# Optimization experiments

Measured on AMD Instinct MI355X. Metric: run time of the kernel, lower is better.

Reference implementation:

```python
import jax, jax.numpy as jnp
import numpy as np

EPS = 1e-5  # haiku LayerNorm default
BIG = 1e9


def layernorm(x, scale, offset):
    mu = jnp.mean(x, axis=-1, keepdims=True)
    var = jnp.var(x, axis=-1, keepdims=True)
    return scale * (x - mu) * jax.lax.rsqrt(var + EPS) + offset


def setup_inputs() -> dict:
    key = jax.random.key(0)
    ks = iter(jax.random.split(key, 32))
    N_res, N_tok, C, H = 4096, 512, 384, 8
    kd = C // H  # 48, key_dim and value_dim per head
    F = 4 * C    # transition hidden
    s = 0.02
    inp = {
        "original": jax.random.normal(next(ks), (1, N_res, C), jnp.float32),
        "resampled": jax.random.normal(next(ks), (1, N_tok, C), jnp.float32),
        "attention_mask": (jax.random.uniform(next(ks), (H, N_tok, N_res)) < 0.9).astype(jnp.float32),
        "output_mask": jnp.ones((1, N_tok), jnp.float32),
        "input_mask": jnp.ones((1, N_res), jnp.float32),
        # cross-attention LayerNorms
        "qn_scale": jnp.ones((C,), jnp.float32), "qn_offset": jnp.zeros((C,), jnp.float32),
        "dn_scale": jnp.ones((C,), jnp.float32), "dn_offset": jnp.zeros((C,), jnp.float32),
        # attention projections
        "query_w": jax.random.normal(next(ks), (C, H, kd), jnp.float32) * s,
        "key_w": jax.random.normal(next(ks), (C, H, kd), jnp.float32) * s,
        "value_w": jax.random.normal(next(ks), (C, H, kd), jnp.float32) * s,
        "gating_w": jax.random.normal(next(ks), (C, H, kd), jnp.float32) * s,
        "gating_b": jnp.ones((H, kd), jnp.float32),
        "output_w": jax.random.normal(next(ks), (H, kd, C), jnp.float32) * s,
        "output_b": jnp.zeros((C,), jnp.float32),
        # resampled transition
        "rt_ln_scale": jnp.ones((C,), jnp.float32), "rt_ln_offset": jnp.zeros((C,), jnp.float32),
        "rt_w1": jax.random.normal(next(ks), (C, F), jnp.float32) * s, "rt_b1": jnp.zeros((F,), jnp.float32),
        "rt_w2": jax.random.normal(next(ks), (F, C), jnp.float32) * s, "rt_b2": jnp.zeros((C,), jnp.float32),
        # original transition
        "ot_ln_scale": jnp.ones((C,), jnp.float32), "ot_ln_offset": jnp.zeros((C,), jnp.float32),
        "ot_w1": jax.random.normal(next(ks), (C, F), jnp.float32) * s, "ot_b1": jnp.zeros((F,), jnp.float32),
        "ot_w2": jax.random.normal(next(ks), (F, C), jnp.float32) * s, "ot_b2": jnp.zeros((C,), jnp.float32),
    }
    return inp


def reference(original, resampled, attention_mask, output_mask, input_mask,
              qn_scale, qn_offset, dn_scale, dn_offset,
              query_w, key_w, value_w, gating_w, gating_b, output_w, output_b,
              rt_ln_scale, rt_ln_offset, rt_w1, rt_b1, rt_w2, rt_b2,
              ot_ln_scale, ot_ln_offset, ot_w1, ot_b1, ot_w2, ot_b2):
    # ---- CrossAttention (deterministic; dropout rate 0) ----
    bias = BIG * (attention_mask - 1.0)          # [H, T, R]
    q_in = layernorm(resampled, qn_scale, qn_offset)   # [1, T, C]
    d_in = layernorm(original, dn_scale, dn_offset)    # [1, R, C]
    kd = query_w.shape[-1]
    q = jnp.einsum('bqa,ahc->bqhc', q_in, query_w) * kd ** (-0.5)
    k = jnp.einsum('bka,ahc->bkhc', d_in, key_w)
    v = jnp.einsum('bka,ahc->bkhc', d_in, value_w)
    logits = jnp.einsum('bqhc,bkhc->bhqk', q, k) + bias[None]  # [1, H, T, R]
    weights = jax.nn.softmax(logits, axis=-1)
    weighted_avg = jnp.einsum('bhqk,bkhc->bqhc', weights, v)
    gate = jax.nn.sigmoid(jnp.einsum('bqc,chv->bqhv', q_in, gating_w) + gating_b)
    weighted_avg = weighted_avg * gate
    attn_out = jnp.einsum('bqhc,hco->bqo', weighted_avg, output_w) + output_b
    resampled = resampled + attn_out             # residual (dropout off)
    # ---- resampled Transition + residual ----
    t = layernorm(resampled, rt_ln_scale, rt_ln_offset)
    t = jax.nn.relu(t @ rt_w1 + rt_b1) @ rt_w2 + rt_b2
    resampled = resampled + t
    # ---- original Transition + residual ----
    t = layernorm(original, ot_ln_scale, ot_ln_offset)
    t = jax.nn.relu(t @ ot_w1 + ot_b1) @ ot_w2 + ot_b2
    original = original + t
    return resampled.astype(jnp.float32), original.astype(jnp.float32)
```

## Files before the change

kernel.cpp:

```cpp
#include <hip/hip_runtime.h>
#include <hip/hip_bf16.h>
#include <cstdint>

typedef unsigned short u16;
typedef __attribute__((ext_vector_type(8))) __bf16 bf16x8;
typedef __attribute__((ext_vector_type(4))) float f32x4;
typedef __attribute__((ext_vector_type(4))) short s16x4;
typedef __attribute__((ext_vector_type(4))) unsigned u32x4;

#define VSTR 4160

__device__ __forceinline__ u16 f2bf(float f) {
  union { float f; unsigned u; } v; v.f = f;
  unsigned r = (v.u + 0x7FFFu + ((v.u >> 16) & 1u)) >> 16;
  return (u16)r;
}

__device__ __forceinline__ void gll16(const u16* gp, u16* lp) {
  auto g1 = reinterpret_cast<const __attribute__((address_space(1))) void*>(
      reinterpret_cast<uintptr_t>(gp));
  auto l3 = reinterpret_cast<__attribute__((address_space(3))) void*>(
      reinterpret_cast<uintptr_t>(lp));
  __builtin_amdgcn_global_load_lds(g1, l3, 16, 0, 0);
}

__global__ __launch_bounds__(256) void mask_bits(const float* __restrict__ mask,
                                                 u16* __restrict__ mb) {
  const int t = blockIdx.x * 256 + threadIdx.x;
  const float* src = mask + (size_t)t * 16;
  unsigned b = 0;
#pragma unroll
  for (int j = 0; j < 4; ++j) {
    const f32x4 v = *(const f32x4*)(src + 4 * j);
#pragma unroll
    for (int k = 0; k < 4; ++k) b |= (v[k] != 0.f ? 1u : 0u) << (4 * j + k);
  }
  mb[t] = (u16)b;
}

__global__ __launch_bounds__(128) void ln_all(
    const float* __restrict__ orig, const float* __restrict__ resam,
    const float* __restrict__ dn_s, const float* __restrict__ dn_o, u16* __restrict__ dinb,
    const float* __restrict__ ot_s, const float* __restrict__ ot_o, u16* __restrict__ otin,
    const float* __restrict__ qn_s, const float* __restrict__ qn_o, u16* __restrict__ qin) {
  const int row = blockIdx.x;
  const int t = threadIdx.x;
  const bool isOrig = row < 4096;
  const float* xr = isOrig ? orig + (size_t)row * 384 : resam + (size_t)(row - 4096) * 384;
  float v0 = xr[t], v1 = xr[t + 128], v2 = xr[t + 256];
  float sum = v0 + v1 + v2;
  float sq = v0 * v0 + v1 * v1 + v2 * v2;
#pragma unroll
  for (int off = 32; off > 0; off >>= 1) {
    sum += __shfl_xor(sum, off);
    sq += __shfl_xor(sq, off);
  }
  __shared__ float red[4];
  if ((t & 63) == 0) { red[(t >> 6) * 2] = sum; red[(t >> 6) * 2 + 1] = sq; }
  __syncthreads();
  sum = red[0] + red[2];
  sq = red[1] + red[3];
  const float mu = sum * (1.f / 384.f);
  const float rstd = rsqrtf(sq * (1.f / 384.f) - mu * mu + 1e-5f);
#pragma unroll
  for (int j = 0; j < 3; ++j) {
    const int cc = t + 128 * j;
    const float xv = (j == 0 ? v0 : (j == 1 ? v1 : v2));
    const float xn = (xv - mu) * rstd;
    if (isOrig) {
      dinb[(size_t)row * 384 + cc] = f2bf(dn_s[cc] * xn + dn_o[cc]);
      otin[(size_t)row * 384 + cc] = f2bf(ot_s[cc] * xn + ot_o[cc]);
    } else {
      qin[(size_t)(row - 4096) * 384 + cc] = f2bf(qn_s[cc] * xn + qn_o[cc]);
    }
  }
}

__global__ __launch_bounds__(128) void ln_kernel(
    const float* __restrict__ x,
    const float* __restrict__ s1, const float* __restrict__ o1, u16* __restrict__ y1) {
  const int row = blockIdx.x;
  const int t = threadIdx.x;
  const float* xr = x + (size_t)row * 384;
  float v0 = xr[t], v1 = xr[t + 128], v2 = xr[t + 256];
  float sum = v0 + v1 + v2;
  float sq = v0 * v0 + v1 * v1 + v2 * v2;
#pragma unroll
  for (int off = 32; off > 0; off >>= 1) {
    sum += __shfl_xor(sum, off);
    sq += __shfl_xor(sq, off);
  }
  __shared__ float red[4];
  if ((t & 63) == 0) { red[(t >> 6) * 2] = sum; red[(t >> 6) * 2 + 1] = sq; }
  __syncthreads();
  sum = red[0] + red[2];
  sq = red[1] + red[3];
  const float mu = sum * (1.f / 384.f);
  const float rstd = rsqrtf(sq * (1.f / 384.f) - mu * mu + 1e-5f);
#pragma unroll
  for (int j = 0; j < 3; ++j) {
    const int cc = t + 128 * j;
    const float xv = (j == 0 ? v0 : (j == 1 ? v1 : v2));
    y1[(size_t)row * 384 + cc] = f2bf(s1[cc] * ((xv - mu) * rstd) + o1[cc]);
  }
}

struct TBatch {
  const float* in[9];
  u16* out[9];
  int K[9], N[9];
  float scale[9];
  int boff[10];
};

__global__ __launch_bounds__(256) void transpose_all(TBatch tb) {
  __shared__ float tile[32][33];
  const int bid = blockIdx.x;
  int j = 0;
  while (j < 8 && bid >= tb.boff[j + 1]) ++j;
  const int lb = bid - tb.boff[j];
  const int NB = tb.N[j] >> 5;
  const int bx = lb % NB, by = lb / NB;
  const float* in = tb.in[j];
  u16* out = tb.out[j];
  const int K = tb.K[j], N = tb.N[j];
  const float scale = tb.scale[j];
  const int tx = threadIdx.x, ty = threadIdx.y;
  const int nb = bx * 32, kb = by * 32;
#pragma unroll
  for (int i = 0; i < 4; ++i)
    tile[ty + 8 * i][tx] = in[(size_t)(kb + ty + 8 * i) * N + nb + tx];
  __syncthreads();
#pragma unroll
  for (int i = 0; i < 4; ++i)
    out[(size_t)(nb + ty + 8 * i) * K + kb + tx] = f2bf(tile[tx][ty + 8 * i] * scale);
}

struct GArgs {
  const u16* A; const u16* Bt;
  int M, N, K, Kld;
  const float* bias; const float* bias2; const float* residual;
  float* outf; u16* outb; u16* outb2;
};

template <int BM, int BN, int EPI>
__global__ __launch_bounds__(256, (BM == 128 ? 2 : 4)) void gemm_bt(GArgs g) {
  constexpr int MT = BM / 32, NT = BN / 32;
  const int tid = threadIdx.x;
  const int w = tid >> 6;
  const int lane = tid & 63;
  const int gq = lane >> 4, c = lane & 15;
  const int brow = blockIdx.y * BM, bcol = blockIdx.x * BN;
  const int wm = (w >> 1) * (BM / 2), wn = (w & 1) * (BN / 2);
  __shared__ u16 As[2][BM][64];
  __shared__ u16 Bs[2][BN][64];
  const int K = g.K;
  const int Kld = g.Kld;
  const size_t koff = (size_t)blockIdx.z * K;

  f32x4 acc[MT][NT];
#pragma unroll
  for (int mt = 0; mt < MT; ++mt)
#pragma unroll
    for (int nt = 0; nt < NT; ++nt)
#pragma unroll
      for (int r = 0; r < 4; ++r) acc[mt][nt][r] = 0.f;

  const int srow = lane >> 3;
  const int schunk = (lane & 7) ^ srow;
  const u16* aSrc = g.A + (size_t)(brow + w * (BM / 4) + srow) * Kld + koff + schunk * 8;
  const u16* bSrc = g.Bt + (size_t)(bcol + w * (BN / 4) + srow) * Kld + koff + schunk * 8;

  auto STAGE = [&](int buf, int k0) {
#pragma unroll
    for (int i = 0; i < BM / 32; ++i)
      gll16(aSrc + (size_t)(8 * i) * Kld + k0, &As[buf][w * (BM / 4) + i * 8][0]);
#pragma unroll
    for (int i = 0; i < BN / 32; ++i)
      gll16(bSrc + (size_t)(8 * i) * Kld + k0, &Bs[buf][w * (BN / 4) + i * 8][0]);
  };

  auto COMPUTE = [&](int buf) {
#pragma unroll
    for (int ks = 0; ks < 2; ++ks) {
      bf16x8 af[MT], bfv[NT];
#pragma unroll
      for (int mt = 0; mt < MT; ++mt) {
        const int row = wm + mt * 16 + c;
        const int ch = ((ks << 2) | gq) ^ (row & 7);
        af[mt] = *(const bf16x8*)&As[buf][row][ch * 8];
      }
#pragma unroll
      for (int nt = 0; nt < NT; ++nt) {
        const int row = wn + nt * 16 + c;
        const int ch = ((ks << 2) | gq) ^ (row & 7);
        bfv[nt] = *(const bf16x8*)&Bs[buf][row][ch * 8];
      }
#pragma unroll
      for (int mt = 0; mt < MT; ++mt)
#pragma unroll
        for (int nt = 0; nt < NT; ++nt)
          acc[mt][nt] =
              __builtin_amdgcn_mfma_f32_16x16x32_bf16(af[mt], bfv[nt], acc[mt][nt], 0, 0, 0);
    }
  };

  const int NTILES = K >> 6;
  STAGE(0, 0);
  __syncthreads();
  int cur = 0;
  for (int t = 0; t < NTILES; ++t) {
    if (t + 1 < NTILES) STAGE(cur ^ 1, (t + 1) << 6);
    COMPUTE(cur);
    __syncthreads();
    cur ^= 1;
  }

  const int N = g.N;
#pragma unroll
  for (int mt = 0; mt < MT; ++mt) {
#pragma unroll
    for (int nt = 0; nt < NT; ++nt) {
      const int n = bcol + wn + nt * 16 + c;
#pragma unroll
      for (int r = 0; r < 4; ++r) {
        const int m = brow + wm + mt * 16 + 4 * gq + r;
        const float v = acc[mt][nt][r];
        if (EPI == 0) {
          g.outb[(size_t)m * N + n] = f2bf(fmaxf(v + g.bias[n], 0.f));
        } else if (EPI == 1) {
          g.outf[(size_t)m * N + n] = v + g.bias[n] + g.residual[(size_t)m * N + n];
        } else if (EPI == 2) {
          if (n < 384)
            g.outb[(size_t)(n / 48) * 4096 * 64 + (size_t)m * 64 + (n % 48)] = f2bf(v);
          else
            g.outb2[(size_t)(n - 384) * VSTR + m] = f2bf(v);
        } else if (EPI == 3) {
          if (n < 384)
            g.outb[(size_t)(n / 48) * 512 * 64 + (size_t)m * 64 + (n % 48)] = f2bf(v);
          else {
            const float sg = v + g.bias2[n - 384];
            g.outf[(size_t)m * 384 + (n - 384)] = 1.f / (1.f + __expf(-sg));
          }
        } else {
          g.outf[(size_t)blockIdx.z * g.M * N + (size_t)m * N + n] = v;
        }
      }
    }
  }
}

__global__ __launch_bounds__(256, 2) void attn_kernel(
    const u16* __restrict__ Kh, const u16* __restrict__ Qb, const u16* __restrict__ Vt,
    const unsigned char* __restrict__ mbits, float* __restrict__ partO,
    float* __restrict__ partL) {
  const int tid = threadIdx.x;
  const int w = tid >> 6;
  const int lane = tid & 63;
  const int gq = lane >> 4, c = lane & 15;
  const int qt = blockIdx.x, h = blockIdx.y, z = blockIdx.z;
  const int tb = qt * 16;
  const int kb = z * 512 + w * 128;

  const u16* qrow = Qb + ((size_t)h * 512 + tb + c) * 64;
  const bf16x8 qf0 = *(const bf16x8*)(qrow + 8 * gq);
  const bf16x8 qf1 = *(const bf16x8*)(qrow + 32 + 8 * gq);

  const u16* kbase = Kh + (size_t)h * 4096 * 64 + (size_t)(kb + c) * 64 + 8 * gq;
  bf16x8 kf[16];
#pragma unroll
  for (int it = 0; it < 4; ++it) {
    const u16* kr = kbase + it * 32 * 64;
    kf[4 * it + 0] = *(const bf16x8*)(kr);
    kf[4 * it + 1] = *(const bf16x8*)(kr + 32);
    kf[4 * it + 2] = *(const bf16x8*)(kr + 16 * 64);
    kf[4 * it + 3] = *(const bf16x8*)(kr + 16 * 64 + 32);
  }

  s16x4 vv[4][3][2];
#pragma unroll
  for (int nt = 0; nt < 3; ++nt) {
    const u16* vc = Vt + ((size_t)h * 48 + nt * 16 + c) * VSTR + kb + 4 * gq;
#pragma unroll
    for (int it = 0; it < 4; ++it) {
      vv[it][nt][0] = *(const s16x4*)(vc + it * 32);
      vv[it][nt][1] = *(const s16x4*)(vc + it * 32 + 16);
    }
  }

  const u32x4 mb =
      *(const u32x4*)(mbits + ((size_t)h * 512 + tb + c) * 512 + (kb >> 3));

  __builtin_amdgcn_sched_barrier(0);

  f32x4 O0, O1, O2;
#pragma unroll
  for (int r = 0; r < 4; ++r) { O0[r] = 0.f; O1[r] = 0.f; O2[r] = 0.f; }
  float psum = 0.f;

#pragma unroll
  for (int it = 0; it < 4; ++it) {
    f32x4 z4;
#pragma unroll
    for (int r = 0; r < 4; ++r) z4[r] = 0.f;
    f32x4 s0 = __builtin_amdgcn_mfma_f32_16x16x32_bf16(kf[4 * it + 0], qf0, z4, 0, 0, 0);
    s0 = __builtin_amdgcn_mfma_f32_16x16x32_bf16(kf[4 * it + 1], qf1, s0, 0, 0, 0);
    f32x4 s1 = __builtin_amdgcn_mfma_f32_16x16x32_bf16(kf[4 * it + 2], qf0, z4, 0, 0, 0);
    s1 = __builtin_amdgcn_mfma_f32_16x16x32_bf16(kf[4 * it + 3], qf1, s1, 0, 0, 0);

    const unsigned wd0 = mb[it] >> (4 * gq);
    const unsigned wd1 = mb[it] >> (16 + 4 * gq);
    float p0[4], p1[4];
#pragma unroll
    for (int r = 0; r < 4; ++r) {
      p0[r] = ((wd0 >> r) & 1u) ? __expf(s0[r]) : 0.f;
      p1[r] = ((wd1 >> r) & 1u) ? __expf(s1[r]) : 0.f;
      psum += p0[r] + p1[r];
    }
    s16x4 pa0, pa1;
    ((unsigned*)&pa0)[0] = __builtin_amdgcn_perm(__builtin_bit_cast(unsigned, p0[1]),
                                                 __builtin_bit_cast(unsigned, p0[0]), 0x07060302u);
    ((unsigned*)&pa0)[1] = __builtin_amdgcn_perm(__builtin_bit_cast(unsigned, p0[3]),
                                                 __builtin_bit_cast(unsigned, p0[2]), 0x07060302u);
    ((unsigned*)&pa1)[0] = __builtin_amdgcn_perm(__builtin_bit_cast(unsigned, p1[1]),
                                                 __builtin_bit_cast(unsigned, p1[0]), 0x07060302u);
    ((unsigned*)&pa1)[1] = __builtin_amdgcn_perm(__builtin_bit_cast(unsigned, p1[3]),
                                                 __builtin_bit_cast(unsigned, p1[2]), 0x07060302u);
    O0 = __builtin_amdgcn_mfma_f32_16x16x16bf16_1k(pa0, vv[it][0][0], O0, 0, 0, 0);
    O0 = __builtin_amdgcn_mfma_f32_16x16x16bf16_1k(pa1, vv[it][0][1], O0, 0, 0, 0);
    O1 = __builtin_amdgcn_mfma_f32_16x16x16bf16_1k(pa0, vv[it][1][0], O1, 0, 0, 0);
    O1 = __builtin_amdgcn_mfma_f32_16x16x16bf16_1k(pa1, vv[it][1][1], O1, 0, 0, 0);
    O2 = __builtin_amdgcn_mfma_f32_16x16x16bf16_1k(pa0, vv[it][2][0], O2, 0, 0, 0);
    O2 = __builtin_amdgcn_mfma_f32_16x16x16bf16_1k(pa1, vv[it][2][1], O2, 0, 0, 0);
  }

  psum += __shfl_xor(psum, 16);
  psum += __shfl_xor(psum, 32);

  __shared__ float oS[4][16][48];
  __shared__ float lS[4][16];
  if (gq == 0) lS[w][c] = psum;
#pragma unroll
  for (int r = 0; r < 4; ++r) {
    oS[w][4 * gq + r][c] = O0[r];
    oS[w][4 * gq + r][16 + c] = O1[r];
    oS[w][4 * gq + r][32 + c] = O2[r];
  }
  __syncthreads();

  float* pO = partO + (((size_t)z * 32 + qt) * 8 + h) * 768;
  for (int idx = tid; idx < 768; idx += 256) {
    const int q = idx / 48, d = idx % 48;
    float v = 0.f;
#pragma unroll
    for (int ww = 0; ww < 4; ++ww) v += oS[ww][q][d];
    pO[idx] = v;
  }
  if (tid < 16) {
    float L = 0.f;
#pragma unroll
    for (int ww = 0; ww < 4; ++ww) L += lS[ww][tid];
    partL[(((size_t)z * 32 + qt) * 8 + h) * 16 + tid] = L;
  }
}

__global__ __launch_bounds__(256) void attn_merge(
    const float* __restrict__ partO, const float* __restrict__ partL,
    const float* __restrict__ gate, u16* __restrict__ attng) {
  const int qt = blockIdx.x, h = blockIdx.y;
  for (int idx = threadIdx.x; idx < 768; idx += 256) {
    const int q = idx / 48, d = idx % 48;
    float O = 0.f, L = 0.f;
#pragma unroll
    for (int z = 0; z < 8; ++z) {
      O += partO[(((size_t)z * 32 + qt) * 8 + h) * 768 + idx];
      L += partL[(((size_t)z * 32 + qt) * 8 + h) * 16 + q];
    }
    const size_t off = (size_t)(qt * 16 + q) * 384 + h * 48 + d;
    attng[off] = f2bf(O / L * gate[off]);
  }
}

__global__ __launch_bounds__(256) void merge_res(
    const float* __restrict__ pT1, const float* __restrict__ res2,
    const float* __restrict__ rtb2, float* __restrict__ out_res) {
  const int i = blockIdx.x * 256 + threadIdx.x;
  const int n0 = (i * 4) % 384;
  f32x4 v = *(const f32x4*)(res2 + (size_t)i * 4);
#pragma unroll
  for (int z = 0; z < 4; ++z) {
    const f32x4 pz = *(const f32x4*)(pT1 + (size_t)z * 512 * 384 + (size_t)i * 4);
#pragma unroll
    for (int r = 0; r < 4; ++r) v[r] += pz[r];
  }
  const f32x4 b = *(const f32x4*)(rtb2 + n0);
#pragma unroll
  for (int r = 0; r < 4; ++r) v[r] += b[r];
  *(f32x4*)(out_res + (size_t)i * 4) = v;
}

extern "C" void kernel_launch(void* const* d_in, const int* in_sizes, int n_in,
                              void* d_out, int out_size, void* d_ws, size_t ws_size,
                              hipStream_t stream) {
  (void)in_sizes; (void)n_in; (void)out_size; (void)ws_size;
  const float* original = (const float*)d_in[0];
  const float* resampled = (const float*)d_in[1];
  const float* amask = (const float*)d_in[2];
  const float* qn_s = (const float*)d_in[5];
  const float* qn_o = (const float*)d_in[6];
  const float* dn_s = (const float*)d_in[7];
  const float* dn_o = (const float*)d_in[8];
  const float* w_q = (const float*)d_in[9];
  const float* w_k = (const float*)d_in[10];
  const float* w_v = (const float*)d_in[11];
  const float* w_g = (const float*)d_in[12];
  const float* b_g = (const float*)d_in[13];
  const float* w_o = (const float*)d_in[14];
  const float* b_o = (const float*)d_in[15];
  const float* rt_s = (const float*)d_in[16];
  const float* rt_o = (const float*)d_in[17];
  const float* rtw1 = (const float*)d_in[18];
  const float* rtb1 = (const float*)d_in[19];
  const float* rtw2 = (const float*)d_in[20];
  const float* rtb2 = (const float*)d_in[21];
  const float* ot_s = (const float*)d_in[22];
  const float* ot_o = (const float*)d_in[23];
  const float* otw1 = (const float*)d_in[24];
  const float* otb1 = (const float*)d_in[25];
  const float* otw2 = (const float*)d_in[26];
  const float* otb2 = (const float*)d_in[27];

  float* out_res = (float*)d_out;
  float* out_orig = out_res + 512 * 384;

  char* p = (char*)d_ws;
  auto alloc = [&](size_t n) {
    void* r = (void*)p;
    p += (n + 255) & ~(size_t)255;
    return r;
  };
  u16* Kh = (u16*)alloc((size_t)8 * 4096 * 64 * 2);
  u16* Qb = (u16*)alloc((size_t)8 * 512 * 64 * 2);
  u16* dinb = (u16*)alloc(4096 * 384 * 2);
  u16* otin = (u16*)alloc(4096 * 384 * 2);
  u16* qin = (u16*)alloc(512 * 384 * 2);
  u16* Vt = (u16*)alloc((size_t)384 * VSTR * 2);
  float* gateb = (float*)alloc(512 * 384 * 4);
  u16* attng = (u16*)alloc(512 * 384 * 2);
  float* res2 = (float*)alloc(512 * 384 * 4);
  u16* tin = (u16*)alloc(512 * 384 * 2);
  u16* H1 = (u16*)alloc(512 * 1536 * 2);
  u16* H2 = (u16*)alloc((size_t)4096 * 1536 * 2);
  float* partT1 = (float*)alloc((size_t)4 * 512 * 384 * 4);
  float* partO = (float*)alloc((size_t)8 * 32 * 8 * 768 * 4);
  float* partL = (float*)alloc((size_t)8 * 32 * 8 * 16 * 4);
  u16* mbitsB = (u16*)alloc((size_t)8 * 512 * 512);
  u16* BtKV = (u16*)alloc(768 * 384 * 2);
  u16* BtQG = (u16*)alloc(768 * 384 * 2);
  u16* OwT = (u16*)alloc(384 * 384 * 2);
  u16* Rt1T = (u16*)alloc(1536 * 384 * 2);
  u16* Rt2T = (u16*)alloc(384 * 1536 * 2);
  u16* Ot1T = (u16*)alloc(1536 * 384 * 2);
  u16* Ot2T = (u16*)alloc(384 * 1536 * 2);

  hipMemsetAsync(Kh, 0, (size_t)8 * 4096 * 64 * 2 + (size_t)8 * 512 * 64 * 2, stream);

  mask_bits<<<4096, 256, 0, stream>>>(amask, mbitsB);

  {
    TBatch tb{};
    const float qscale = 0.14433756729740643f;
    const float* ins[9] = {w_q, w_g, w_k, w_v, w_o, rtw1, rtw2, otw1, otw2};
    u16* outs[9] = {BtQG, BtQG + 384 * 384, BtKV, BtKV + 384 * 384, OwT,
                    Rt1T, Rt2T, Ot1T, Ot2T};
    const int Ks[9] = {384, 384, 384, 384, 384, 384, 1536, 384, 1536};
    const int Ns[9] = {384, 384, 384, 384, 384, 1536, 384, 1536, 384};
    int off = 0;
    for (int j = 0; j < 9; ++j) {
      tb.in[j] = ins[j]; tb.out[j] = outs[j];
      tb.K[j] = Ks[j]; tb.N[j] = Ns[j];
      tb.scale[j] = (j == 0) ? qscale : 1.f;
      tb.boff[j] = off;
      off += (Ns[j] >> 5) * (Ks[j] >> 5);
    }
    tb.boff[9] = off;
    transpose_all<<<off, dim3(32, 8), 0, stream>>>(tb);
  }

  ln_all<<<4608, 128, 0, stream>>>(original, resampled, dn_s, dn_o, dinb,
                                   ot_s, ot_o, otin, qn_s, qn_o, qin);

  {
    GArgs a{};
    a.A = dinb; a.Bt = BtKV; a.M = 4096; a.N = 768; a.K = 384; a.Kld = 384;
    a.outb = Kh; a.outb2 = Vt;
    gemm_bt<128, 128, 2><<<dim3(6, 32), 256, 0, stream>>>(a);
  }
  {
    GArgs a{};
    a.A = qin; a.Bt = BtQG; a.M = 512; a.N = 768; a.K = 384; a.Kld = 384;
    a.outb = Qb; a.outf = gateb; a.bias2 = b_g;
    gemm_bt<64, 64, 3><<<dim3(12, 8), 256, 0, stream>>>(a);
  }

  attn_kernel<<<dim3(32, 8, 8), 256, 0, stream>>>(
      Kh, Qb, Vt, (const unsigned char*)mbitsB, partO, partL);
  attn_merge<<<dim3(32, 8), 256, 0, stream>>>(partO, partL, gateb, attng);

  {
    GArgs a{};
    a.A = attng; a.Bt = OwT; a.M = 512; a.N = 384; a.K = 384; a.Kld = 384;
    a.bias = b_o; a.residual = resampled; a.outf = res2;
    gemm_bt<64, 64, 1><<<dim3(6, 8), 256, 0, stream>>>(a);
  }
  ln_kernel<<<512, 128, 0, stream>>>(res2, rt_s, rt_o, tin);
  {
    GArgs a{};
    a.A = tin; a.Bt = Rt1T; a.M = 512; a.N = 1536; a.K = 384; a.Kld = 384;
    a.bias = rtb1; a.outb = H1;
    gemm_bt<64, 64, 0><<<dim3(24, 8), 256, 0, stream>>>(a);
  }
  {
    GArgs a{};
    a.A = H1; a.Bt = Rt2T; a.M = 512; a.N = 384; a.K = 384; a.Kld = 1536;
    a.outf = partT1;
    gemm_bt<64, 64, 4><<<dim3(6, 8, 4), 256, 0, stream>>>(a);
  }
  {
    GArgs a{};
    a.A = otin; a.Bt = Ot1T; a.M = 4096; a.N = 1536; a.K = 384; a.Kld = 384;
    a.bias = otb1; a.outb = H2;
    gemm_bt<128, 128, 0><<<dim3(12, 32), 256, 0, stream>>>(a);
  }
  {
    GArgs a{};
    a.A = H2; a.Bt = Ot2T; a.M = 4096; a.N = 384; a.K = 1536; a.Kld = 1536;
    a.bias = otb2; a.residual = original; a.outf = out_orig;
    gemm_bt<64, 64, 1><<<dim3(6, 64), 256, 0, stream>>>(a);
  }
  merge_res<<<192, 256, 0, stream>>>(partT1, res2, rtb2, out_res);
}
```

Measured before the change: 291.7 us.

## Share K/V tiles in LDS across four query tiles in attention kernel

The attention kernel changes from one query tile per block with keys split across waves to four query tiles per block (one per wave) sharing double-buffered, XOR-swizzled K and V chunks staged in LDS via global_load_lds. Each K/V chunk is now read from global memory once per four query tiles, and the cross-wave LDS reduction of partial outputs goes away. The cost is a serial four-chunk loop with block barriers and a quarter as many blocks. Separately, the KV-projection and original-transition first GEMMs switch to 128x64 tiles, doubling their grid sizes.

```diff
diff --git a/kernel.cpp b/kernel.cpp
--- a/kernel.cpp
+++ b/kernel.cpp
@@ -258,110 +258,119 @@
   const int w = tid >> 6;
   const int lane = tid & 63;
   const int gq = lane >> 4, c = lane & 15;
-  const int qt = blockIdx.x, h = blockIdx.y, z = blockIdx.z;
-  const int tb = qt * 16;
-  const int kb = z * 512 + w * 128;
-
-  const u16* qrow = Qb + ((size_t)h * 512 + tb + c) * 64;
+  const int qg = blockIdx.x, h = blockIdx.y, z = blockIdx.z;
+  const int qt = qg * 4 + w;
+  const int kb = z * 512;
+
+  __shared__ u16 Ks[2][128][64];
+  __shared__ u16 Vs[2][48][128];
+
+  const u16* qrow = Qb + ((size_t)h * 512 + qt * 16 + c) * 64;
   const bf16x8 qf0 = *(const bf16x8*)(qrow + 8 * gq);
   const bf16x8 qf1 = *(const bf16x8*)(qrow + 32 + 8 * gq);
 
-  const u16* kbase = Kh + (size_t)h * 4096 * 64 + (size_t)(kb + c) * 64 + 8 * gq;
-  bf16x8 kf[16];
-#pragma unroll
-  for (int it = 0; it < 4; ++it) {
-    const u16* kr = kbase + it * 32 * 64;
-    kf[4 * it + 0] = *(const bf16x8*)(kr);
-    kf[4 * it + 1] = *(const bf16x8*)(kr + 32);
-    kf[4 * it + 2] = *(const bf16x8*)(kr + 16 * 64);
-    kf[4 * it + 3] = *(const bf16x8*)(kr + 16 * 64 + 32);
-  }
-
-  s16x4 vv[4][3][2];
-#pragma unroll
-  for (int nt = 0; nt < 3; ++nt) {
-    const u16* vc = Vt + ((size_t)h * 48 + nt * 16 + c) * VSTR + kb + 4 * gq;
-#pragma unroll
-    for (int it = 0; it < 4; ++it) {
-      vv[it][nt][0] = *(const s16x4*)(vc + it * 32);
-      vv[it][nt][1] = *(const s16x4*)(vc + it * 32 + 16);
-    }
-  }
-
-  const u32x4 mb =
-      *(const u32x4*)(mbits + ((size_t)h * 512 + tb + c) * 512 + (kb >> 3));
-
-  __builtin_amdgcn_sched_barrier(0);
+  const unsigned char* mrow = mbits + ((size_t)h * 512 + qt * 16 + c) * 512 + z * 64;
+  u32x4 mbAll[4];
+#pragma unroll
+  for (int ch = 0; ch < 4; ++ch) mbAll[ch] = *(const u32x4*)(mrow + ch * 16);
+
+  const int krow8 = lane >> 3;
+  const int kch = (lane & 7) ^ krow8;
+  const u16* kbase = Kh + (size_t)h * 4096 * 64;
+  const int vrow4 = lane >> 4;
+  const int vk16 = lane & 15;
+
+  auto STAGE = [&](int buf, int ch) {
+    const int k0 = kb + ch * 128;
+#pragma unroll
+    for (int j = 0; j < 4; ++j) {
+      const int row = w * 32 + j * 8 + krow8;
+      gll16(kbase + (size_t)(k0 + row) * 64 + kch * 8, &Ks[buf][w * 32 + j * 8][0]);
+    }
+#pragma unroll
+    for (int j = 0; j < 3; ++j) {
+      const int d = w * 12 + j * 4 + vrow4;
+      const int sk = vk16 ^ (d & 15);
+      gll16(Vt + (size_t)(h * 48 + d) * VSTR + k0 + sk * 8, &Vs[buf][w * 12 + j * 4][0]);
+    }
+  };
 
   f32x4 O0, O1, O2;
 #pragma unroll
   for (int r = 0; r < 4; ++r) { O0[r] = 0.f; O1[r] = 0.f; O2[r] = 0.f; }
   float psum = 0.f;
-
-#pragma unroll
-  for (int it = 0; it < 4; ++it) {
-    f32x4 z4;
-#pragma unroll
-    for (int r = 0; r < 4; ++r) z4[r] = 0.f;
-    f32x4 s0 = __builtin_amdgcn_mfma_f32_16x16x32_bf16(kf[4 * it + 0], qf0, z4, 0, 0, 0);
-    s0 = __builtin_amdgcn_mfma_f32_16x16x32_bf16(kf[4 * it + 1], qf1, s0, 0, 0, 0);
-    f32x4 s1 = __builtin_amdgcn_mfma_f32_16x16x32_bf16(kf[4 * it + 2], qf0, z4, 0, 0, 0);
-    s1 = __builtin_amdgcn_mfma_f32_16x16x32_bf16(kf[4 * it + 3], qf1, s1, 0, 0, 0);
-
-    const unsigned wd0 = mb[it] >> (4 * gq);
-    const unsigned wd1 = mb[it] >> (16 + 4 * gq);
-    float p0[4], p1[4];
-#pragma unroll
-    for (int r = 0; r < 4; ++r) {
-      p0[r] = ((wd0 >> r) & 1u) ? __expf(s0[r]) : 0.f;
-      p1[r] = ((wd1 >> r) & 1u) ? __expf(s1[r]) : 0.f;
-      psum += p0[r] + p1[r];
-    }
-    s16x4 pa0, pa1;
-    ((unsigned*)&pa0)[0] = __builtin_amdgcn_perm(__builtin_bit_cast(unsigned, p0[1]),
-                                                 __builtin_bit_cast(unsigned, p0[0]), 0x07060302u);
-    ((unsigned*)&pa0)[1] = __builtin_amdgcn_perm(__builtin_bit_cast(unsigned, p0[3]),
-                                                 __builtin_bit_cast(unsigned, p0[2]), 0x07060302u);
-    ((unsigned*)&pa1)[0] = __builtin_amdgcn_perm(__builtin_bit_cast(unsigned, p1[1]),
-                                                 __builtin_bit_cast(unsigned, p1[0]), 0x07060302u);
-    ((unsigned*)&pa1)[1] = __builtin_amdgcn_perm(__builtin_bit_cast(unsigned, p1[3]),
-                                                 __builtin_bit_cast(unsigned, p1[2]), 0x07060302u);
-    O0 = __builtin_amdgcn_mfma_f32_16x16x16bf16_1k(pa0, vv[it][0][0], O0, 0, 0, 0);
-    O0 = __builtin_amdgcn_mfma_f32_16x16x16bf16_1k(pa1, vv[it][0][1], O0, 0, 0, 0);
-    O1 = __builtin_amdgcn_mfma_f32_16x16x16bf16_1k(pa0, vv[it][1][0], O1, 0, 0, 0);
-    O1 = __builtin_amdgcn_mfma_f32_16x16x16bf16_1k(pa1, vv[it][1][1], O1, 0, 0, 0);
-    O2 = __builtin_amdgcn_mfma_f32_16x16x16bf16_1k(pa0, vv[it][2][0], O2, 0, 0, 0);
-    O2 = __builtin_amdgcn_mfma_f32_16x16x16bf16_1k(pa1, vv[it][2][1], O2, 0, 0, 0);
+  f32x4 z4;
+#pragma unroll
+  for (int r = 0; r < 4; ++r) z4[r] = 0.f;
+
+  STAGE(0, 0);
+  __syncthreads();
+  int cur = 0;
+  for (int ch = 0; ch < 4; ++ch) {
+    if (ch + 1 < 4) STAGE(cur ^ 1, ch + 1);
+#pragma unroll
+    for (int s = 0; s < 4; ++s) {
+      const int keyA = s * 32 + c;
+      const int keyB = keyA + 16;
+      const bf16x8 kA0 = *(const bf16x8*)&Ks[cur][keyA][(gq ^ (keyA & 7)) * 8];
+      const bf16x8 kA1 = *(const bf16x8*)&Ks[cur][keyA][((4 + gq) ^ (keyA & 7)) * 8];
+      const bf16x8 kB0 = *(const bf16x8*)&Ks[cur][keyB][(gq ^ (keyB & 7)) * 8];
+      const bf16x8 kB1 = *(const bf16x8*)&Ks[cur][keyB][((4 + gq) ^ (keyB & 7)) * 8];
+
+      f32x4 s0 = __builtin_amdgcn_mfma_f32_16x16x32_bf16(kA0, qf0, z4, 0, 0, 0);
+      s0 = __builtin_amdgcn_mfma_f32_16x16x32_bf16(kA1, qf1, s0, 0, 0, 0);
+      f32x4 s1 = __builtin_amdgcn_mfma_f32_16x16x32_bf16(kB0, qf0, z4, 0, 0, 0);
+      s1 = __builtin_amdgcn_mfma_f32_16x16x32_bf16(kB1, qf1, s1, 0, 0, 0);
+
+      const unsigned word = mbAll[ch][s];
+      const unsigned wd0 = word >> (4 * gq);
+      const unsigned wd1 = word >> (16 + 4 * gq);
+      float p0[4], p1[4];
+#pragma unroll
+      for (int r = 0; r < 4; ++r) {
+        p0[r] = ((wd0 >> r) & 1u) ? __expf(s0[r]) : 0.f;
+        p1[r] = ((wd1 >> r) & 1u) ? __expf(s1[r]) : 0.f;
+        psum += p0[r] + p1[r];
+      }
+      s16x4 pa0, pa1;
+      ((unsigned*)&pa0)[0] = __builtin_amdgcn_perm(__builtin_bit_cast(unsigned, p0[1]),
+                                                   __builtin_bit_cast(unsigned, p0[0]), 0x07060302u);
+      ((unsigned*)&pa0)[1] = __builtin_amdgcn_perm(__builtin_bit_cast(unsigned, p0[3]),
+                                                   __builtin_bit_cast(unsigned, p0[2]), 0x07060302u);
+      ((unsigned*)&pa1)[0] = __builtin_amdgcn_perm(__builtin_bit_cast(unsigned, p1[1]),
+                                                   __builtin_bit_cast(unsigned, p1[0]), 0x07060302u);
+      ((unsigned*)&pa1)[1] = __builtin_amdgcn_perm(__builtin_bit_cast(unsigned, p1[3]),
+                                                   __builtin_bit_cast(unsigned, p1[2]), 0x07060302u);
+
+#pragma unroll
+      for (int nt = 0; nt < 3; ++nt) {
+        const int row = nt * 16 + c;
+        const int klA = s * 32 + 4 * gq;
+        const int klB = klA + 16;
+        const s16x4 vfA = *(const s16x4*)&Vs[cur][row][(((klA >> 3) ^ c) << 3) + (gq & 1) * 4];
+        const s16x4 vfB = *(const s16x4*)&Vs[cur][row][(((klB >> 3) ^ c) << 3) + (gq & 1) * 4];
+        f32x4& O = (nt == 0 ? O0 : (nt == 1 ? O1 : O2));
+        O = __builtin_amdgcn_mfma_f32_16x16x16bf16_1k(pa0, vfA, O, 0, 0, 0);
+        O = __builtin_amdgcn_mfma_f32_16x16x16bf16_1k(pa1, vfB, O, 0, 0, 0);
+      }
+    }
+    __syncthreads();
+    cur ^= 1;
   }
 
   psum += __shfl_xor(psum, 16);
   psum += __shfl_xor(psum, 32);
 
-  __shared__ float oS[4][16][48];
-  __shared__ float lS[4][16];
-  if (gq == 0) lS[w][c] = psum;
+  float* pO = partO + (((size_t)z * 32 + qt) * 8 + h) * 768;
 #pragma unroll
   for (int r = 0; r < 4; ++r) {
-    oS[w][4 * gq + r][c] = O0[r];
-    oS[w][4 * gq + r][16 + c] = O1[r];
-    oS[w][4 * gq + r][32 + c] = O2[r];
-  }
-  __syncthreads();
-
-  float* pO = partO + (((size_t)z * 32 + qt) * 8 + h) * 768;
-  for (int idx = tid; idx < 768; idx += 256) {
-    const int q = idx / 48, d = idx % 48;
-    float v = 0.f;
-#pragma unroll
-    for (int ww = 0; ww < 4; ++ww) v += oS[ww][q][d];
-    pO[idx] = v;
-  }
-  if (tid < 16) {
-    float L = 0.f;
-#pragma unroll
-    for (int ww = 0; ww < 4; ++ww) L += lS[ww][tid];
-    partL[(((size_t)z * 32 + qt) * 8 + h) * 16 + tid] = L;
-  }
+    const int q = 4 * gq + r;
+    pO[q * 48 + c] = O0[r];
+    pO[q * 48 + 16 + c] = O1[r];
+    pO[q * 48 + 32 + c] = O2[r];
+  }
+  if (gq == 0)
+    partL[(((size_t)z * 32 + qt) * 8 + h) * 16 + c] = psum;
 }
 
 __global__ __launch_bounds__(256) void attn_merge(
@@ -494,7 +503,7 @@
     GArgs a{};
     a.A = dinb; a.Bt = BtKV; a.M = 4096; a.N = 768; a.K = 384; a.Kld = 384;
     a.outb = Kh; a.outb2 = Vt;
-    gemm_bt<128, 128, 2><<<dim3(6, 32), 256, 0, stream>>>(a);
+    gemm_bt<128, 64, 2><<<dim3(12, 32), 256, 0, stream>>>(a);
   }
   {
     GArgs a{};
@@ -503,7 +512,7 @@
     gemm_bt<64, 64, 3><<<dim3(12, 8), 256, 0, stream>>>(a);
   }
 
-  attn_kernel<<<dim3(32, 8, 8), 256, 0, stream>>>(
+  attn_kernel<<<dim3(8, 8, 8), 256, 0, stream>>>(
       Kh, Qb, Vt, (const unsigned char*)mbitsB, partO, partL);
   attn_merge<<<dim3(32, 8), 256, 0, stream>>>(partO, partL, gateb, attng);
 
@@ -530,7 +539,7 @@
     GArgs a{};
     a.A = otin; a.Bt = Ot1T; a.M = 4096; a.N = 1536; a.K = 384; a.Kld = 384;
     a.bias = otb1; a.outb = H2;
-    gemm_bt<128, 128, 0><<<dim3(12, 32), 256, 0, stream>>>(a);
+    gemm_bt<128, 64, 0><<<dim3(24, 32), 256, 0, stream>>>(a);
   }
   {
     GArgs a{};
```

Result: faster. 261.3 us (-10.4%).
